# Kernel optimization log

Measured on AMD Instinct MI355X. Metric: run time of the kernel, lower is better.

## Reference

```python
import jax, jax.numpy as jnp
import numpy as np

NUM_REL = 50000
NUM_EDGES = 1000000
DIM_IN = 128
DIM_OUT = 128
NUM_HEAD = 8
DIM_HID = DIM_OUT // NUM_HEAD


def setup_inputs() -> dict:
    key = jax.random.key(0)
    ks = jax.random.split(key, 5)
    emb_rel = jax.random.normal(ks[0], (NUM_REL, DIM_IN), dtype=jnp.float32)
    relation_triplets = jax.random.randint(ks[1], (NUM_EDGES, 3), 0, NUM_REL, dtype=jnp.int64)
    # xavier-normal-ish scales
    attn_w = jax.random.normal(ks[2], (DIM_OUT, 2 * DIM_IN), dtype=jnp.float32) * np.sqrt(2.0 / (DIM_OUT + 2 * DIM_IN))
    attn_b = jnp.zeros((DIM_OUT,), dtype=jnp.float32)
    attn_vec = jax.random.normal(ks[3], (1, NUM_HEAD, DIM_HID), dtype=jnp.float32) * np.sqrt(2.0 / (NUM_HEAD + DIM_HID))
    aggr_w = jax.random.normal(ks[4], (DIM_OUT, DIM_IN), dtype=jnp.float32) * np.sqrt(2.0 / (DIM_OUT + DIM_IN))
    aggr_b = jnp.zeros((DIM_OUT,), dtype=jnp.float32)
    return {"emb_rel": emb_rel, "relation_triplets": relation_triplets,
            "attn_w": attn_w, "attn_b": attn_b, "attn_vec": attn_vec,
            "aggr_w": aggr_w, "aggr_b": aggr_b}


def reference(emb_rel, relation_triplets, attn_w, attn_b, attn_vec, aggr_w, aggr_b):
    num_rel = emb_rel.shape[0]
    head = relation_triplets[:, 0]
    tail = relation_triplets[:, 1]
    h = emb_rel[head]                         # [E, Din]
    t = emb_rel[tail]                         # [E, Din]
    concat = jnp.concatenate([h, t], axis=-1) # [E, 2*Din]
    # per-edge attention logits
    a = jnp.tanh(concat @ attn_w.T + attn_b).reshape(-1, NUM_HEAD, DIM_HID)
    raw = jnp.sum(a * attn_vec, axis=-1)      # [E, H]
    # segment softmax over edges grouped by head relation
    m = jax.ops.segment_max(raw, head, num_segments=num_rel)   # [R, H]
    ev = jnp.exp(raw - m[head])                                # [E, H]
    s = jax.ops.segment_sum(ev, head, num_segments=num_rel)    # [R, H]
    beta = ev / (s[head] + 1e-16)                              # [E, H]
    # weighted aggregation of projected tail embeddings
    msg = (t @ aggr_w.T + aggr_b).reshape(-1, NUM_HEAD, DIM_HID)  # [E, H, Dh]
    out = jax.ops.segment_sum(beta[..., None] * msg, head, num_segments=num_rel)
    return out.reshape(num_rel, NUM_HEAD * DIM_HID)
```

## Files before the change

kernel.cpp:

```cpp
#include <hip/hip_runtime.h>
#include <hip/hip_bf16.h>

#define DIM 128
#define NHEAD 8
#define CAP_B 64
#define NPART 8
#define CAP8 20
#define MAXD 64

typedef __attribute__((ext_vector_type(8))) short short8;
typedef __attribute__((ext_vector_type(4))) float f32x4;
typedef __attribute__((ext_vector_type(4))) int int4v;

__device__ __forceinline__ unsigned short f2bf(float x) {
    unsigned u = __float_as_uint(x);
    unsigned r = (u + 0x7fffu + ((u >> 16) & 1)) >> 16;
    return (unsigned short)r;
}
__device__ __forceinline__ float bf_lo(unsigned v) { return __uint_as_float(v << 16); }
__device__ __forceinline__ float bf_hi(unsigned v) { return __uint_as_float(v & 0xffff0000u); }

__device__ __forceinline__ float fast_tanh(float x) {
    float e = __expf(2.f * x);
    return 1.f - 2.f * __builtin_amdgcn_rcpf(e + 1.f);
}

__global__ __launch_bounds__(256) void partition_kernel(
    const int4v* __restrict__ trip4, unsigned* __restrict__ binbuf,
    int* __restrict__ blockcnt,
    const float* __restrict__ attn_w, const float* __restrict__ aggr_w,
    unsigned short* __restrict__ w16,
    int nE, int nbP1, int BINS)
{
    if ((int)blockIdx.x >= nbP1) {
        int f = (blockIdx.x - nbP1) * 256 + threadIdx.x;
        if (f >= 3 * 128 * 16) return;
        int m   = f / 2048;
        int rem = f - m * 2048;
        int gc  = rem >> 4;
        int k8  = (rem & 15) * 8;
        const float* src = (m == 2) ? &aggr_w[(size_t)gc * 128 + k8]
                                    : &attn_w[(size_t)gc * 256 + m * 128 + k8];
        float4 v0 = *(const float4*)src;
        float4 v1 = *(const float4*)(src + 4);
        short8 r;
        r[0] = (short)f2bf(v0.x); r[1] = (short)f2bf(v0.y);
        r[2] = (short)f2bf(v0.z); r[3] = (short)f2bf(v0.w);
        r[4] = (short)f2bf(v1.x); r[5] = (short)f2bf(v1.y);
        r[6] = (short)f2bf(v1.z); r[7] = (short)f2bf(v1.w);
        *(short8*)&w16[(size_t)f * 8] = r;
        return;
    }

    __shared__ int hist[64];
    __shared__ int base[64];
    __shared__ int tot;
    __shared__ unsigned recs[1024];
    const int tid = threadIdx.x;
    if (tid < 64) hist[tid] = 0;
    __syncthreads();

    int i = blockIdx.x * 256 + tid;
    int e0 = i * 4;
    int h[4] = {-1, -1, -1, -1}, t[4] = {0, 0, 0, 0};
    if (e0 + 3 < nE) {
        int4v v0 = __builtin_nontemporal_load(&trip4[(size_t)i * 3 + 0]);
        int4v v1 = __builtin_nontemporal_load(&trip4[(size_t)i * 3 + 1]);
        int4v v2 = __builtin_nontemporal_load(&trip4[(size_t)i * 3 + 2]);
        h[0] = v0.x; t[0] = v0.y; h[1] = v0.w; t[1] = v1.x;
        h[2] = v1.z; t[2] = v1.w; h[3] = v2.y; t[3] = v2.z;
    } else if (e0 < nE) {
        const int* trip = (const int*)trip4;
#pragma unroll
        for (int j = 0; j < 4; ++j)
            if (e0 + j < nE) { h[j] = trip[(size_t)(e0 + j) * 3]; t[j] = trip[(size_t)(e0 + j) * 3 + 1]; }
    }

    int bn[4], ofs[4];
#pragma unroll
    for (int j = 0; j < 4; ++j) {
        if (h[j] >= 0) {
            bn[j]  = h[j] >> 10;
            ofs[j] = atomicAdd(&hist[bn[j]], 1);
        }
    }
    __syncthreads();

    if (tid < 64) {
        int v = hist[tid];
        int x = v;
#pragma unroll
        for (int d = 1; d < 64; d <<= 1) {
            int y = __shfl_up(x, d);
            if (tid >= d) x += y;
        }
        base[tid] = x - v;
        if (tid == 63) tot = x;
    }
    __syncthreads();

#pragma unroll
    for (int j = 0; j < 4; ++j)
        if (h[j] >= 0) recs[base[bn[j]] + ofs[j]] = ((unsigned)h[j] << 16) | (unsigned)t[j];
    __syncthreads();

    const int total = tot;
    for (int idx = tid; idx < total; idx += 256) {
        unsigned r = recs[idx];
        int b    = (int)(r >> 26);
        int slot = idx - base[b];
        if (slot < CAP_B)
            binbuf[((size_t)b * nbP1 + blockIdx.x) * CAP_B + slot] = r;
    }
    if (tid < BINS) blockcnt[(size_t)tid * nbP1 + blockIdx.x] = min(hist[tid], CAP_B);
}

__global__ __launch_bounds__(256) void scatter_mfma_kernel(
    const unsigned* __restrict__ binbuf, const int* __restrict__ blockcnt,
    unsigned short* __restrict__ bucket8,
    int* __restrict__ count8,
    const float* __restrict__ emb,
    const unsigned short* __restrict__ w16,
    const float* __restrict__ attn_b,
    const float* __restrict__ aggr_b,
    unsigned short* __restrict__ hW16,
    unsigned short* __restrict__ twm,
    int nR, int nbP1, int nbBS)
{
    __shared__ int lcnt[1024];
    __shared__ unsigned short stag[1024 * CAP8];
    __shared__ short bcs[1024];

    if ((int)blockIdx.x < nbBS) {
        const int tid  = threadIdx.x;
        const int b    = blockIdx.x >> 3;
        const int part = blockIdx.x & (NPART - 1);
        const int hbase = b << 10;

        for (int j = tid; j < 1024; j += 256) lcnt[j] = 0;
        for (int j = tid; j < nbP1; j += 256) bcs[j] = (short)blockcnt[(size_t)b * nbP1 + j];
        __syncthreads();

        const int nSeg = (nbP1 > part) ? (nbP1 - part + NPART - 1) / NPART : 0;
        const int totSlots = nSeg * CAP_B;
        for (int f = tid; f < totSlots; f += 256) {
            int k = f >> 6;
            int s = f & 63;
            int j = part + NPART * k;
            if (s < (int)bcs[j]) {
                unsigned r = binbuf[((size_t)b * nbP1 + j) * CAP_B + s];
                int rel  = (int)(r >> 16) - hbase;
                int slot = atomicAdd(&lcnt[rel], 1);
                if (slot < CAP8) stag[rel * CAP8 + slot] = (unsigned short)(r & 0xffffu);
            }
        }
        __syncthreads();

        unsigned* dstw = (unsigned*)(bucket8 + ((size_t)part * nR + hbase) * CAP8);
        const unsigned* srcw = (const unsigned*)stag;
        const int nHead = min(1024, nR - hbase);
        const int nW = nHead * (CAP8 / 2);
        for (int j = tid; j < nW; j += 256) dstw[j] = srcw[j];
        for (int rel = tid; rel < nHead; rel += 256)
            count8[(size_t)part * nR + hbase + rel] = min(lcnt[rel], CAP8);
        return;
    }

    const int vb   = blockIdx.x - nbBS;
    const int row0 = vb * 64;
    const int wave = threadIdx.x >> 6;
    const int lane = threadIdx.x & 63;
    const int lrow = lane & 15;
    const int kg   = lane >> 4;
    const int kbase = kg * 8;
    const int R = nR;

    short8 a[4][4];
#pragma unroll
    for (int rt = 0; rt < 4; ++rt) {
        int r = row0 + rt * 16 + lrow;
        const float* arow = &emb[(size_t)(r < R ? r : R - 1) * 128];
#pragma unroll
        for (int kk = 0; kk < 4; ++kk) {
            float4 v0 = *(const float4*)&arow[kk * 32 + kbase];
            float4 v1 = *(const float4*)&arow[kk * 32 + kbase + 4];
            short8 av;
            av[0] = (short)f2bf(v0.x); av[1] = (short)f2bf(v0.y);
            av[2] = (short)f2bf(v0.z); av[3] = (short)f2bf(v0.w);
            av[4] = (short)f2bf(v1.x); av[5] = (short)f2bf(v1.y);
            av[6] = (short)f2bf(v1.z); av[7] = (short)f2bf(v1.w);
            a[rt][kk] = av;
        }
    }

    for (int m = 0; m < 3; ++m) {
#pragma unroll
        for (int ct2 = 0; ct2 < 2; ++ct2) {
            const int gc = (wave * 2 + ct2) * 16 + lrow;
            const unsigned short* wrow = &w16[((size_t)m * 128 + gc) * 128];
            f32x4 acc[4];
#pragma unroll
            for (int rt = 0; rt < 4; ++rt) acc[rt] = (f32x4){0.f, 0.f, 0.f, 0.f};
#pragma unroll
            for (int kk = 0; kk < 4; ++kk) {
                short8 bfr = *(const short8*)&wrow[kk * 32 + kbase];
#pragma unroll
                for (int rt = 0; rt < 4; ++rt)
                    acc[rt] = __builtin_amdgcn_mfma_f32_16x16x32_bf16(a[rt][kk], bfr, acc[rt], 0, 0, 0);
            }
            float bv = (m == 0) ? attn_b[gc] : ((m == 2) ? aggr_b[gc] : 0.f);
#pragma unroll
            for (int rt = 0; rt < 4; ++rt) {
#pragma unroll
                for (int reg = 0; reg < 4; ++reg) {
                    int gr = row0 + rt * 16 + kg * 4 + reg;
                    if (gr < R) {
                        unsigned short val = f2bf(acc[rt][reg] + bv);
                        if (m == 0) {
                            hW16[(size_t)gr * 128 + gc] = val;
                        } else {
                            twm[(size_t)gr * 256 + (gc >> 1) * 4 + (gc & 1) + ((m == 2) ? 2 : 0)] = val;
                        }
                    }
                }
            }
        }
    }
}

__global__ __launch_bounds__(256) void head_fused_kernel(
    const int* __restrict__ count8,
    const unsigned short* __restrict__ bucket8,
    const unsigned* __restrict__ hW16,
    const unsigned* __restrict__ twm,
    const float* __restrict__ attn_vec,
    float* __restrict__ out,
    int nR)
{
    const int w    = threadIdx.x >> 6;
    const int h    = blockIdx.x * 4 + w;
    if (h >= nR) return;
    const int lane = threadIdx.x & 63;
    const int d0 = lane * 2;

    const float2 av = *(const float2*)&attn_vec[d0];

    int cv = (lane < NPART) ? min(count8[(size_t)lane * nR + h], CAP8) : 0;
    int c[NPART];
#pragma unroll
    for (int j = 0; j < NPART; ++j) c[j] = __shfl(cv, j);
    int cnt = 0;
#pragma unroll
    for (int j = 0; j < NPART; ++j) cnt += c[j];
    cnt = min(cnt, MAXD);

    float s = 0.f, acc0 = 0.f, acc1 = 0.f;

    if (cnt > 0) {
        unsigned vh = hW16[(unsigned)h * 64u + lane];
        const float hx = bf_lo(vh), hy = bf_hi(vh);

        float A = fabsf(av.x) + fabsf(av.y);
        A += __shfl_xor(A, 1);
        A += __shfl_xor(A, 2);
        A += __shfl_xor(A, 4);
        const float m = A;

        int idx = min(lane, cnt - 1);
        int x = 0, p = 0, P = 0;
#pragma unroll
        for (int j = 0; j < NPART - 1; ++j) {
            P += c[j];
            bool go = idx >= P;
            x = go ? j + 1 : x;
            p = go ? P : p;
        }
        int myt = (int)bucket8[((unsigned)x * (unsigned)nR + (unsigned)h) * CAP8 + (unsigned)(idx - p)];

        const unsigned loff = (unsigned)lane * 2u;
        int i = 0;
        for (; i + 4 <= cnt; i += 4) {
            int t0 = __shfl(myt, i),     t1 = __shfl(myt, i + 1);
            int t2 = __shfl(myt, i + 2), t3 = __shfl(myt, i + 3);
            uint2 v0 = *(const uint2*)(twm + ((unsigned)t0 * 128u + loff));
            uint2 v1 = *(const uint2*)(twm + ((unsigned)t1 * 128u + loff));
            uint2 v2 = *(const uint2*)(twm + ((unsigned)t2 * 128u + loff));
            uint2 v3 = *(const uint2*)(twm + ((unsigned)t3 * 128u + loff));

            float p0 = fast_tanh(hx + bf_lo(v0.x)) * av.x + fast_tanh(hy + bf_hi(v0.x)) * av.y;
            float p1 = fast_tanh(hx + bf_lo(v1.x)) * av.x + fast_tanh(hy + bf_hi(v1.x)) * av.y;
            float p2 = fast_tanh(hx + bf_lo(v2.x)) * av.x + fast_tanh(hy + bf_hi(v2.x)) * av.y;
            float p3 = fast_tanh(hx + bf_lo(v3.x)) * av.x + fast_tanh(hy + bf_hi(v3.x)) * av.y;
            p0 += __shfl_xor(p0, 1); p1 += __shfl_xor(p1, 1);
            p2 += __shfl_xor(p2, 1); p3 += __shfl_xor(p3, 1);
            p0 += __shfl_xor(p0, 2); p1 += __shfl_xor(p1, 2);
            p2 += __shfl_xor(p2, 2); p3 += __shfl_xor(p3, 2);
            p0 += __shfl_xor(p0, 4); p1 += __shfl_xor(p1, 4);
            p2 += __shfl_xor(p2, 4); p3 += __shfl_xor(p3, 4);

            float e0 = __expf(p0 - m), e1 = __expf(p1 - m);
            float e2 = __expf(p2 - m), e3 = __expf(p3 - m);
            s += (e0 + e1) + (e2 + e3);
            acc0 += e0 * bf_lo(v0.y) + e1 * bf_lo(v1.y) + e2 * bf_lo(v2.y) + e3 * bf_lo(v3.y);
            acc1 += e0 * bf_hi(v0.y) + e1 * bf_hi(v1.y) + e2 * bf_hi(v2.y) + e3 * bf_hi(v3.y);
        }
        for (; i < cnt; ++i) {
            int t0 = __shfl(myt, i);
            uint2 v0 = *(const uint2*)(twm + ((unsigned)t0 * 128u + loff));
            float p0 = fast_tanh(hx + bf_lo(v0.x)) * av.x + fast_tanh(hy + bf_hi(v0.x)) * av.y;
            p0 += __shfl_xor(p0, 1);
            p0 += __shfl_xor(p0, 2);
            p0 += __shfl_xor(p0, 4);
            float e0 = __expf(p0 - m);
            s += e0;
            acc0 += e0 * bf_lo(v0.y);
            acc1 += e0 * bf_hi(v0.y);
        }
    }

    float inv = 1.f / (s + 1e-16f);
    float2 o; o.x = acc0 * inv; o.y = acc1 * inv;
    *(float2*)&out[(size_t)h * 128 + d0] = o;
}

extern "C" void kernel_launch(void* const* d_in, const int* in_sizes, int n_in,
                              void* d_out, int out_size, void* d_ws, size_t ws_size,
                              hipStream_t stream) {
    const float* emb      = (const float*)d_in[0];
    const int*   trip     = (const int*)d_in[1];
    const float* attn_w   = (const float*)d_in[2];
    const float* attn_b   = (const float*)d_in[3];
    const float* attn_vec = (const float*)d_in[4];
    const float* aggr_w   = (const float*)d_in[5];
    const float* aggr_b   = (const float*)d_in[6];
    float*       out      = (float*)d_out;

    const int nR   = in_sizes[0] / DIM;
    const int nE   = in_sizes[1] / 3;
    const int nbP1 = (nE + 1023) / 1024;
    const int BINS = (nR + 1023) >> 10;
    const int nbW  = (3 * 128 * 16 + 255) / 256;
    const int nbBS = BINS * NPART;
    const int nbMM = (nR + 63) / 64;

    unsigned short* hW16    = (unsigned short*)d_ws;
    unsigned short* twm     = hW16 + (size_t)nR * 128;
    unsigned short* w16     = twm + (size_t)nR * 256;
    unsigned short* bucket8 = w16 + (size_t)3 * 128 * 128;
    int*            count8  = (int*)(bucket8 + (size_t)NPART * nR * CAP8);
    unsigned*       binbuf  = (unsigned*)(count8 + (size_t)NPART * nR);
    int*            blockcnt= (int*)(binbuf + (size_t)BINS * nbP1 * CAP_B);

    partition_kernel<<<nbP1 + nbW, 256, 0, stream>>>(
        (const int4v*)trip, binbuf, blockcnt, attn_w, aggr_w, w16, nE, nbP1, BINS);
    scatter_mfma_kernel<<<nbBS + nbMM, 256, 0, stream>>>(
        binbuf, blockcnt, bucket8, count8,
        emb, w16, attn_b, aggr_b, hW16, twm, nR, nbP1, nbBS);
    head_fused_kernel<<<(nR + 3) / 4, 256, 0, stream>>>(
        count8, bucket8, (const unsigned*)hW16, (const unsigned*)twm,
        attn_vec, out, nR);
}
```

Baseline: 132.8 us.

## Precompute per-node tanh and use the tanh addition identity per edge

Applies tanh to the head and tail projections once per relation in the MFMA stage and stores them as fp32. Each edge logit is then formed with the identity tanh(a+b) = (ta+tb)/(1+ta*tb), using one reciprocal instead of two exps and two reciprocals per element. The message projection moves to a separate bf16 array. This cuts transcendental work in the edge loop but doubles the bytes gathered per edge for the tail attention term (fp32 instead of bf16) and splits one gather into two, which may raise memory traffic.

```diff
diff --git a/kernel.cpp b/kernel.cpp
--- a/kernel.cpp
+++ b/kernel.cpp
@@ -7,6 +7,7 @@
 #define NPART 8
 #define CAP8 20
 #define MAXD 64
+#define L2E 1.4426950408889634f
 
 typedef __attribute__((ext_vector_type(8))) short short8;
 typedef __attribute__((ext_vector_type(4))) float f32x4;
@@ -20,9 +21,10 @@
 __device__ __forceinline__ float bf_lo(unsigned v) { return __uint_as_float(v << 16); }
 __device__ __forceinline__ float bf_hi(unsigned v) { return __uint_as_float(v & 0xffff0000u); }
 
-__device__ __forceinline__ float fast_tanh(float x) {
+__device__ __forceinline__ float tanh_clamp(float x) {
     float e = __expf(2.f * x);
-    return 1.f - 2.f * __builtin_amdgcn_rcpf(e + 1.f);
+    float v = 1.f - 2.f * __builtin_amdgcn_rcpf(e + 1.f);
+    return fminf(0.999999f, fmaxf(-0.999999f, v));
 }
 
 __global__ __launch_bounds__(256) void partition_kernel(
@@ -123,8 +125,9 @@
     const unsigned short* __restrict__ w16,
     const float* __restrict__ attn_b,
     const float* __restrict__ aggr_b,
-    unsigned short* __restrict__ hW16,
-    unsigned short* __restrict__ twm,
+    float* __restrict__ thW,
+    float* __restrict__ tt32,
+    unsigned short* __restrict__ msg16,
     int nR, int nbP1, int nbBS)
 {
     __shared__ int lcnt[1024];
@@ -215,12 +218,10 @@
                 for (int reg = 0; reg < 4; ++reg) {
                     int gr = row0 + rt * 16 + kg * 4 + reg;
                     if (gr < R) {
-                        unsigned short val = f2bf(acc[rt][reg] + bv);
-                        if (m == 0) {
-                            hW16[(size_t)gr * 128 + gc] = val;
-                        } else {
-                            twm[(size_t)gr * 256 + (gc >> 1) * 4 + (gc & 1) + ((m == 2) ? 2 : 0)] = val;
-                        }
+                        float val = acc[rt][reg] + bv;
+                        if (m == 0)      thW [(size_t)gr * 128 + gc] = tanh_clamp(val);
+                        else if (m == 1) tt32[(size_t)gr * 128 + gc] = tanh_clamp(val);
+                        else             msg16[(size_t)gr * 128 + gc] = f2bf(val);
                     }
                 }
             }
@@ -231,8 +232,9 @@
 __global__ __launch_bounds__(256) void head_fused_kernel(
     const int* __restrict__ count8,
     const unsigned short* __restrict__ bucket8,
-    const unsigned* __restrict__ hW16,
-    const unsigned* __restrict__ twm,
+    const float* __restrict__ thW,
+    const float* __restrict__ tt32,
+    const unsigned* __restrict__ msg16,
     const float* __restrict__ attn_vec,
     float* __restrict__ out,
     int nR)
@@ -257,14 +259,13 @@
     float s = 0.f, acc0 = 0.f, acc1 = 0.f;
 
     if (cnt > 0) {
-        unsigned vh = hW16[(unsigned)h * 64u + lane];
-        const float hx = bf_lo(vh), hy = bf_hi(vh);
+        const float2 th = *(const float2*)(thW + (size_t)h * 128 + d0);
 
         float A = fabsf(av.x) + fabsf(av.y);
         A += __shfl_xor(A, 1);
         A += __shfl_xor(A, 2);
         A += __shfl_xor(A, 4);
-        const float m = A;
+        const float qm = A * L2E;
 
         int idx = min(lane, cnt - 1);
         int x = 0, p = 0, P = 0;
@@ -277,20 +278,27 @@
         }
         int myt = (int)bucket8[((unsigned)x * (unsigned)nR + (unsigned)h) * CAP8 + (unsigned)(idx - p)];
 
-        const unsigned loff = (unsigned)lane * 2u;
         int i = 0;
         for (; i + 4 <= cnt; i += 4) {
             int t0 = __shfl(myt, i),     t1 = __shfl(myt, i + 1);
             int t2 = __shfl(myt, i + 2), t3 = __shfl(myt, i + 3);
-            uint2 v0 = *(const uint2*)(twm + ((unsigned)t0 * 128u + loff));
-            uint2 v1 = *(const uint2*)(twm + ((unsigned)t1 * 128u + loff));
-            uint2 v2 = *(const uint2*)(twm + ((unsigned)t2 * 128u + loff));
-            uint2 v3 = *(const uint2*)(twm + ((unsigned)t3 * 128u + loff));
-
-            float p0 = fast_tanh(hx + bf_lo(v0.x)) * av.x + fast_tanh(hy + bf_hi(v0.x)) * av.y;
-            float p1 = fast_tanh(hx + bf_lo(v1.x)) * av.x + fast_tanh(hy + bf_hi(v1.x)) * av.y;
-            float p2 = fast_tanh(hx + bf_lo(v2.x)) * av.x + fast_tanh(hy + bf_hi(v2.x)) * av.y;
-            float p3 = fast_tanh(hx + bf_lo(v3.x)) * av.x + fast_tanh(hy + bf_hi(v3.x)) * av.y;
+            float2 a0 = *(const float2*)(tt32 + (unsigned)t0 * 128u + d0);
+            float2 a1 = *(const float2*)(tt32 + (unsigned)t1 * 128u + d0);
+            float2 a2 = *(const float2*)(tt32 + (unsigned)t2 * 128u + d0);
+            float2 a3 = *(const float2*)(tt32 + (unsigned)t3 * 128u + d0);
+            unsigned q0 = msg16[(unsigned)t0 * 64u + lane];
+            unsigned q1 = msg16[(unsigned)t1 * 64u + lane];
+            unsigned q2 = msg16[(unsigned)t2 * 64u + lane];
+            unsigned q3 = msg16[(unsigned)t3 * 64u + lane];
+
+            float p0 = (th.x + a0.x) * __builtin_amdgcn_rcpf(fmaf(th.x, a0.x, 1.f)) * av.x
+                     + (th.y + a0.y) * __builtin_amdgcn_rcpf(fmaf(th.y, a0.y, 1.f)) * av.y;
+            float p1 = (th.x + a1.x) * __builtin_amdgcn_rcpf(fmaf(th.x, a1.x, 1.f)) * av.x
+                     + (th.y + a1.y) * __builtin_amdgcn_rcpf(fmaf(th.y, a1.y, 1.f)) * av.y;
+            float p2 = (th.x + a2.x) * __builtin_amdgcn_rcpf(fmaf(th.x, a2.x, 1.f)) * av.x
+                     + (th.y + a2.y) * __builtin_amdgcn_rcpf(fmaf(th.y, a2.y, 1.f)) * av.y;
+            float p3 = (th.x + a3.x) * __builtin_amdgcn_rcpf(fmaf(th.x, a3.x, 1.f)) * av.x
+                     + (th.y + a3.y) * __builtin_amdgcn_rcpf(fmaf(th.y, a3.y, 1.f)) * av.y;
             p0 += __shfl_xor(p0, 1); p1 += __shfl_xor(p1, 1);
             p2 += __shfl_xor(p2, 1); p3 += __shfl_xor(p3, 1);
             p0 += __shfl_xor(p0, 2); p1 += __shfl_xor(p1, 2);
@@ -298,23 +306,27 @@
             p0 += __shfl_xor(p0, 4); p1 += __shfl_xor(p1, 4);
             p2 += __shfl_xor(p2, 4); p3 += __shfl_xor(p3, 4);
 
-            float e0 = __expf(p0 - m), e1 = __expf(p1 - m);
-            float e2 = __expf(p2 - m), e3 = __expf(p3 - m);
+            float e0 = exp2f(fmaf(p0, L2E, -qm));
+            float e1 = exp2f(fmaf(p1, L2E, -qm));
+            float e2 = exp2f(fmaf(p2, L2E, -qm));
+            float e3 = exp2f(fmaf(p3, L2E, -qm));
             s += (e0 + e1) + (e2 + e3);
-            acc0 += e0 * bf_lo(v0.y) + e1 * bf_lo(v1.y) + e2 * bf_lo(v2.y) + e3 * bf_lo(v3.y);
-            acc1 += e0 * bf_hi(v0.y) + e1 * bf_hi(v1.y) + e2 * bf_hi(v2.y) + e3 * bf_hi(v3.y);
+            acc0 += e0 * bf_lo(q0) + e1 * bf_lo(q1) + e2 * bf_lo(q2) + e3 * bf_lo(q3);
+            acc1 += e0 * bf_hi(q0) + e1 * bf_hi(q1) + e2 * bf_hi(q2) + e3 * bf_hi(q3);
         }
         for (; i < cnt; ++i) {
             int t0 = __shfl(myt, i);
-            uint2 v0 = *(const uint2*)(twm + ((unsigned)t0 * 128u + loff));
-            float p0 = fast_tanh(hx + bf_lo(v0.x)) * av.x + fast_tanh(hy + bf_hi(v0.x)) * av.y;
+            float2 a0 = *(const float2*)(tt32 + (unsigned)t0 * 128u + d0);
+            unsigned q0 = msg16[(unsigned)t0 * 64u + lane];
+            float p0 = (th.x + a0.x) * __builtin_amdgcn_rcpf(fmaf(th.x, a0.x, 1.f)) * av.x
+                     + (th.y + a0.y) * __builtin_amdgcn_rcpf(fmaf(th.y, a0.y, 1.f)) * av.y;
             p0 += __shfl_xor(p0, 1);
             p0 += __shfl_xor(p0, 2);
             p0 += __shfl_xor(p0, 4);
-            float e0 = __expf(p0 - m);
+            float e0 = exp2f(fmaf(p0, L2E, -qm));
             s += e0;
-            acc0 += e0 * bf_lo(v0.y);
-            acc1 += e0 * bf_hi(v0.y);
+            acc0 += e0 * bf_lo(q0);
+            acc1 += e0 * bf_hi(q0);
         }
     }
 
@@ -343,9 +355,10 @@
     const int nbBS = BINS * NPART;
     const int nbMM = (nR + 63) / 64;
 
-    unsigned short* hW16    = (unsigned short*)d_ws;
-    unsigned short* twm     = hW16 + (size_t)nR * 128;
-    unsigned short* w16     = twm + (size_t)nR * 256;
+    float*          thW     = (float*)d_ws;
+    float*          tt32    = thW + (size_t)nR * 128;
+    unsigned short* msg16   = (unsigned short*)(tt32 + (size_t)nR * 128);
+    unsigned short* w16     = msg16 + (size_t)nR * 128;
     unsigned short* bucket8 = w16 + (size_t)3 * 128 * 128;
     int*            count8  = (int*)(bucket8 + (size_t)NPART * nR * CAP8);
     unsigned*       binbuf  = (unsigned*)(count8 + (size_t)NPART * nR);
@@ -355,8 +368,7 @@
         (const int4v*)trip, binbuf, blockcnt, attn_w, aggr_w, w16, nE, nbP1, BINS);
     scatter_mfma_kernel<<<nbBS + nbMM, 256, 0, stream>>>(
         binbuf, blockcnt, bucket8, count8,
-        emb, w16, attn_b, aggr_b, hW16, twm, nR, nbP1, nbBS);
+        emb, w16, attn_b, aggr_b, thW, tt32, msg16, nR, nbP1, nbBS);
     head_fused_kernel<<<(nR + 3) / 4, 256, 0, stream>>>(
-        count8, bucket8, (const unsigned*)hW16, (const unsigned*)twm,
-        attn_vec, out, nR);
-}
+        count8, bucket8, thW, tt32, (const unsigned*)msg16, attn_vec, out, nR);
+}
```

Measured after the change: 166.2 us. 1.25x slower.
